# Optimization experiments

Hardware: AMD Instinct MI355X
Metric: run time of the kernel (lower is better)

Reference implementation:

```python
import jax, jax.numpy as jnp
import numpy as np

V_SIZE, E, H = 30000, 256, 128   # vocab, emb_dim, GRU hidden per direction
B, U, T, ND = 32, 32, 128, 64    # dialogues, utterances, max tokens, dialogue-id table size
SCALE = E ** 0.5                  # attention normalise_factor = hid_size**0.5, hid_size = emb_dim


def _gru_dir(x_seq, w_ih, w_hh, b_ih, b_hh):
    """Unidirectional torch-style GRU. x_seq: [N,T,E] -> [N,T,H]."""
    xp = jnp.einsum('nte,ge->ntg', x_seq, w_ih) + b_ih   # precompute input gates [N,T,3H]
    xp = jnp.swapaxes(xp, 0, 1)                          # [T,N,3H]

    def step(h, xpt):
        gh = h @ w_hh.T + b_hh
        r = jax.nn.sigmoid(xpt[:, :H] + gh[:, :H])
        z = jax.nn.sigmoid(xpt[:, H:2 * H] + gh[:, H:2 * H])
        n = jnp.tanh(xpt[:, 2 * H:] + r * gh[:, 2 * H:])
        h_new = (1.0 - z) * n + z * h
        return h_new, h_new

    h0 = jnp.zeros((x_seq.shape[0], H), x_seq.dtype)
    _, out = jax.lax.scan(step, h0, xp)
    return jnp.swapaxes(out, 0, 1)


def _forward(x, d_ids, utt_len, emb_table,
             w_ih_f, w_hh_f, b_ih_f, b_hh_f,
             w_ih_b, w_hh_b, b_ih_b, b_hh_b,
             wq, bq, wk, bk, wv, bv, wo, bo, wl, bl):
    b, u, t = x.shape
    N = b * u
    emb = emb_table[x.reshape(N, t)]                      # [N,T,E]
    lens = jnp.clip(utt_len[d_ids].reshape(N), 1, t)      # valid tokens per utterance
    pos = jnp.arange(t)
    # index map that reverses the valid prefix (padding region clipped, unused)
    rev_idx = jnp.clip(lens[:, None] - 1 - pos[None, :], 0, t - 1)  # [N,T]

    o_f = _gru_dir(emb, w_ih_f, w_hh_f, b_ih_f, b_hh_f)   # causal => correct on valid prefix
    emb_rev = jnp.take_along_axis(emb, rev_idx[:, :, None], axis=1)
    o_b = jnp.take_along_axis(_gru_dir(emb_rev, w_ih_b, w_hh_b, b_ih_b, b_hh_b),
                              rev_idx[:, :, None], axis=1)
    h = jnp.concatenate([o_f, o_b], axis=-1)              # [N,T,E] bi-GRU states

    # self-attention pooling; original takes op[-1], so only the query at the
    # last valid token (lens-1) is needed -- identical math, less compute.
    k = jnp.einsum('nte,he->nth', h, wk) + bk
    v = jnp.einsum('nte,he->nth', h, wv) + bv
    h_last = jnp.take_along_axis(h, (lens - 1)[:, None, None], axis=1)[:, 0]  # [N,E]
    q = h_last @ wq.T + bq
    score = jnp.einsum('nh,nth->nt', q, k) / SCALE
    score = jnp.where(pos[None, :] < lens[:, None], score, -jnp.inf)
    attn = jax.nn.softmax(score, axis=-1)
    ctx = jnp.einsum('nt,nth->nh', attn, v)
    out = (ctx @ wo.T + bo) @ wl.T + bl                   # make_output then final linear
    return out.reshape(b, u, -1)


def setup_inputs() -> dict:
    key = jax.random.key(0)
    ks = jax.random.split(key, 16)

    def p(k, shape):
        return (jax.random.normal(k, shape, jnp.float32) / np.sqrt(shape[-1])).astype(jnp.float32)

    return {
        'x': jax.random.randint(ks[0], (B, U, T), 0, V_SIZE, dtype=jnp.int32),
        'd_ids': jax.random.randint(ks[1], (B,), 0, ND, dtype=jnp.int32),
        'utt_len': jax.random.randint(ks[2], (ND, U), 1, T + 1, dtype=jnp.int32),
        'emb_table': p(ks[3], (V_SIZE, E)),
        'w_ih_f': p(ks[4], (3 * H, E)), 'w_hh_f': p(ks[5], (3 * H, H)),
        'b_ih_f': jnp.zeros(3 * H, jnp.float32), 'b_hh_f': jnp.zeros(3 * H, jnp.float32),
        'w_ih_b': p(ks[6], (3 * H, E)), 'w_hh_b': p(ks[7], (3 * H, H)),
        'b_ih_b': jnp.zeros(3 * H, jnp.float32), 'b_hh_b': jnp.zeros(3 * H, jnp.float32),
        'wq': p(ks[8], (E, E)), 'bq': jnp.zeros(E, jnp.float32),
        'wk': p(ks[9], (E, E)), 'bk': jnp.zeros(E, jnp.float32),
        'wv': p(ks[10], (E, E)), 'bv': jnp.zeros(E, jnp.float32),
        'wo': p(ks[11], (E, E)), 'bo': jnp.zeros(E, jnp.float32),
        'wl': p(ks[12], (E, E)), 'bl': jnp.zeros(E, jnp.float32),
    }


def reference(x, d_ids, utt_len, emb_table,
              w_ih_f, w_hh_f, b_ih_f, b_hh_f,
              w_ih_b, w_hh_b, b_ih_b, b_hh_b,
              wq, bq, wk, bk, wv, bv, wo, bo, wl, bl):
    return _forward(x, d_ids, utt_len, emb_table,
                    w_ih_f, w_hh_f, b_ih_f, b_hh_f,
                    w_ih_b, w_hh_b, b_ih_b, b_hh_b,
                    wq, bq, wk, bk, wv, bv, wo, bo, wl, bl)
```

## Files before the change

### kernel.cpp

```cpp
#include <hip/hip_runtime.h>
#include <hip/hip_bf16.h>
#include <math.h>
#include <stdint.h>

typedef unsigned short u16;
typedef unsigned int   u32;
typedef __attribute__((ext_vector_type(8))) short bf16x8;
typedef __attribute__((ext_vector_type(4))) float f32x4;

#define EDIM 256
#define HDIM 128
#define TLEN 128
#define NUTT 1024
#define UU   32
#define NBU  8

#define WS_FLAG 0
#define WS_LENS 64
#define WS_TAB  4608
#define WS_COPY 8192
#define WS_OF   18874368LL
#define WS_OB   52428800LL

#define MFMA16(a, b, c) __builtin_amdgcn_mfma_f32_16x16x32_bf16((a), (b), (c), 0, 0, 0)
#define SOUT(u, s, j) ((u) * 1096 + (s) * 136 + (j))

__constant__ int G_SZ[18] = {7680000, 98304, 49152, 384, 384, 98304, 49152, 384, 384,
                             65536, 256, 65536, 65536, 256, 65536, 256, 65536, 256};

__device__ __forceinline__ float b2f(u16 b) {
    u32 u = ((u32)b) << 16; float f; __builtin_memcpy(&f, &u, 4); return f;
}
__device__ __forceinline__ u16 f2b(float f) {
    u32 u; __builtin_memcpy(&u, &f, 4);
    u32 r = u + 0x7FFFu + ((u >> 16) & 1u);
    return (u16)(r >> 16);
}
__device__ __forceinline__ u16 f2b_hw(float f) {
    __hip_bfloat16 h = __float2bfloat16(f);
    u16 v; __builtin_memcpy(&v, &h, 2); return v;
}
__device__ __forceinline__ float fsigmoid(float x) { return 1.0f / (1.0f + __expf(-x)); }
__device__ __forceinline__ float ftanh(float x) { return 1.0f - 2.0f / (__expf(2.0f * x) + 1.0f); }

__global__ __launch_bounds__(256)
void k_convert(void* ws,
               const int* __restrict__ d_ids, const int* __restrict__ utt_len,
               const void* a0, const void* a1, const void* a2, const void* a3,
               const void* a4, const void* a5, const void* a6, const void* a7,
               const void* a8, const void* a9, const void* a10, const void* a11,
               const void* a12, const void* a13, const void* a14, const void* a15,
               const void* a16, const void* a17) {
    __shared__ int scnt[4];
    const int tid = threadIdx.x, lane = tid & 63, wid = tid >> 6;
    const u16* p = (const u16*)a0;
    int cnt = 0;
#pragma unroll 8
    for (int i = tid; i < 16384; i += 256)
        cnt += ((p[i] & 0x7F80) == 0x7F80) ? 1 : 0;
#pragma unroll
    for (int o = 32; o > 0; o >>= 1) cnt += __shfl_down(cnt, o);
    if (lane == 0) scnt[wid] = cnt;
    __syncthreads();
    const int flag = (scnt[0] + scnt[1] + scnt[2] + scnt[3] > 0) ? 1 : 0;

    if (blockIdx.x == 0) {
        if (tid == 0) {
            const void* orig[18] = {a0,a1,a2,a3,a4,a5,a6,a7,a8,a9,a10,a11,a12,a13,a14,a15,a16,a17};
            *(int*)((char*)ws + WS_FLAG) = flag;
            const u16** tab = (const u16**)((char*)ws + WS_TAB);
            char* base = (char*)ws + WS_COPY;
            long long cum = 0;
            for (int a = 0; a < 18; ++a) {
                tab[a] = flag ? (const u16*)(base + cum * 2) : (const u16*)orig[a];
                cum += G_SZ[a];
            }
        }
        int* lens = (int*)((char*)ws + WS_LENS);
#pragma unroll 4
        for (int n = tid; n < NUTT; n += 256) {
            int b = n >> 5;
            int u = n & (UU - 1);
            int L = utt_len[d_ids[b] * UU + u];
            lens[n] = min(max(L, 1), TLEN);
        }
    }

    if (flag == 0) return;
    const void* orig[18] = {a0,a1,a2,a3,a4,a5,a6,a7,a8,a9,a10,a11,a12,a13,a14,a15,a16,a17};
    u16* base = (u16*)((char*)ws + WS_COPY);
    const int gtid = blockIdx.x * blockDim.x + tid;
    const int gs   = gridDim.x * blockDim.x;
    long long cum = 0;
    for (int a = 0; a < 18; ++a) {
        const float4* src = (const float4*)orig[a];
        uint2* dst = (uint2*)(base + cum);
        const int n4 = G_SZ[a] >> 2;
        for (int i = gtid; i < n4; i += gs) {
            float4 v = src[i];
            uint2 pk;
            pk.x = (u32)f2b(v.x) | ((u32)f2b(v.y) << 16);
            pk.y = (u32)f2b(v.z) | ((u32)f2b(v.w) << 16);
            dst[i] = pk;
        }
        cum += G_SZ[a];
    }
}

__global__ __launch_bounds__(512)
void k_scan(const int* __restrict__ x, void* ws) {
    const u16* const* tab = (const u16* const*)((char*)ws + WS_TAB);
    const int dir = blockIdx.y;
    const u16* emb  = tab[0];
    const u16* w_ih = tab[1 + dir * 4];
    const u16* w_hh = tab[2 + dir * 4];
    const u16* b_ih = tab[3 + dir * 4];
    const u16* b_hh = tab[4 + dir * 4];
    u16* outp = (u16*)((char*)ws + (dir ? WS_OB : WS_OF));
    const int* lens = (const int*)((char*)ws + WS_LENS);

    const int n0 = blockIdx.x * NBU;
    __shared__ __align__(16) u16 sh_emb[2][NBU][264];
    __shared__ __align__(16) u16 sh_hi[2][NBU * 136];
    __shared__ __align__(16) u16 sh_lo[2][NBU * 136];
    __shared__ __align__(16) u16 sh_out[2][NBU * 1096];
    __shared__ int sh_tok[NBU * TLEN];
    __shared__ int sh_L[NBU];

    const int tid = threadIdx.x, lane = tid & 63, wvi = tid >> 6;
    const int q4 = lane >> 4, mm = lane & 15;
    const int j = wvi * 16 + mm;
    const int u8 = mm & 7;

    for (int i = tid; i < NBU * 136; i += 512) { sh_hi[0][i] = 0; sh_lo[0][i] = 0; }
    for (int i = tid; i < NBU * TLEN; i += 512) {
        const int u = i >> 7, tt = i & 127;
        sh_tok[i] = x[(n0 + u) * TLEN + tt];
    }
    if (tid < NBU) sh_L[tid] = lens[n0 + tid];

    bf16x8 wih[3][8]; bf16x8 whh[3][4];
    float bcr, bcz, bxn, bgn;
#pragma unroll
    for (int n3 = 0; n3 < 3; ++n3) {
        const int g = n3 * HDIM + j;
#pragma unroll
        for (int ks = 0; ks < 8; ++ks)
            wih[n3][ks] = *(const bf16x8*)(w_ih + g * EDIM + ks * 32 + q4 * 8);
#pragma unroll
        for (int ks = 0; ks < 4; ++ks)
            whh[n3][ks] = *(const bf16x8*)(w_hh + g * HDIM + ks * 32 + q4 * 8);
    }
    bcr = b2f(b_ih[j]) + b2f(b_hh[j]);
    bcz = b2f(b_ih[HDIM + j]) + b2f(b_hh[HDIM + j]);
    bxn = b2f(b_ih[2 * HDIM + j]);
    bgn = b2f(b_hh[2 * HDIM + j]);

    const int arr0 = (q4 & 2);
    float hprev[2] = {0.f, 0.f};
    const f32x4 zero4 = {0.f, 0.f, 0.f, 0.f};
    __syncthreads();

    const bool pwave = (wvi < 4);
    const int pf_u = lane & 7;
    const int pf_c = wvi * 8 + (lane >> 3);
    const int pf_L = sh_L[pf_u];

    uint4 pf;
    if (pwave) {
        const int te0 = dir ? (pf_L - 1) : 0;
        const int tok = sh_tok[pf_u * TLEN + te0];
        pf = *(const uint4*)(emb + (size_t)tok * EDIM + pf_c * 8);
        *(uint4*)&sh_emb[0][pf_u][pf_c * 8] = pf;
    }
    __syncthreads();

    for (int t = 0; t < TLEN; ++t) {
        const int cur = t & 1, nxt = cur ^ 1;
        const int obuf = (t >> 3) & 1, slot = t & 7;

        if (pwave && (t + 1 < TLEN)) {
            const int te = dir ? max(pf_L - 2 - t, 0) : (t + 1);
            const int tok = sh_tok[pf_u * TLEN + te];
            pf = *(const uint4*)(emb + (size_t)tok * EDIM + pf_c * 8);
        }

        f32x4 accx[3], accg[3];
        {
            bf16x8 a = *(const bf16x8*)&sh_emb[cur][u8][q4 * 8];
#pragma unroll
            for (int n3 = 0; n3 < 3; ++n3) accx[n3] = MFMA16(a, wih[n3][0], zero4);
        }
#pragma unroll
        for (int ks = 1; ks < 8; ++ks) {
            bf16x8 a = *(const bf16x8*)&sh_emb[cur][u8][ks * 32 + q4 * 8];
#pragma unroll
            for (int n3 = 0; n3 < 3; ++n3) accx[n3] = MFMA16(a, wih[n3][ks], accx[n3]);
        }
        {
            bf16x8 ahi = *(const bf16x8*)(sh_hi[cur] + u8 * 136 + q4 * 8);
            bf16x8 alo = *(const bf16x8*)(sh_lo[cur] + u8 * 136 + q4 * 8);
#pragma unroll
            for (int n3 = 0; n3 < 3; ++n3) {
                accg[n3] = MFMA16(ahi, whh[n3][0], zero4);
                accg[n3] = MFMA16(alo, whh[n3][0], accg[n3]);
            }
        }
#pragma unroll
        for (int ks = 1; ks < 4; ++ks) {
            bf16x8 ahi = *(const bf16x8*)(sh_hi[cur] + u8 * 136 + ks * 32 + q4 * 8);
            bf16x8 alo = *(const bf16x8*)(sh_lo[cur] + u8 * 136 + ks * 32 + q4 * 8);
#pragma unroll
            for (int n3 = 0; n3 < 3; ++n3) {
                accg[n3] = MFMA16(ahi, whh[n3][ks], accg[n3]);
                accg[n3] = MFMA16(alo, whh[n3][ks], accg[n3]);
            }
        }

#pragma unroll
        for (int rr2 = 0; rr2 < 2; ++rr2) {
            const int arr = rr2 + arr0;
            const int u   = (q4 * 4 + arr) & 7;
            const float r  = fsigmoid(accx[0][arr] + accg[0][arr] + bcr);
            const float z  = fsigmoid(accx[1][arr] + accg[1][arr] + bcz);
            const float nn = ftanh((accx[2][arr] + bxn) + r * (accg[2][arr] + bgn));
            const float hn = (1.0f - z) * nn + z * hprev[rr2];
            hprev[rr2] = hn;
            const u16 hb = f2b_hw(hn);
            sh_hi[nxt][u * 136 + j] = hb;
            sh_lo[nxt][u * 136 + j] = f2b_hw(hn - b2f(hb));
            sh_out[obuf][SOUT(u, slot, j)] = hb;
        }

        if (pwave && (t + 1 < TLEN))
            *(uint4*)&sh_emb[nxt][pf_u][pf_c * 8] = pf;

        __syncthreads();

        if (slot == 7) {
            const int rowIdx = tid >> 3;
            const int part   = tid & 7;
            const int fu = rowIdx >> 3, fs = rowIdx & 7;
            const int tt = (t & ~7) + fs;
            const int tout = dir ? (sh_L[fu] - 1 - tt) : tt;
            if (tout >= 0) {
                const u16* srcp = &sh_out[obuf][SOUT(fu, fs, part * 16)];
                uint4 v0 = *(const uint4*)(srcp);
                uint4 v1 = *(const uint4*)(srcp + 8);
                u16* dstp = outp + ((size_t)(n0 + fu) * TLEN + tout) * HDIM + part * 16;
                *(uint4*)(dstp)     = v0;
                *(uint4*)(dstp + 8) = v1;
            }
        }
    }
}

__global__ __launch_bounds__(256)
void k_attn(void* ws, void* outv) {
    const u16* const* tab = (const u16* const*)((char*)ws + WS_TAB);
    const u16* wq = tab[9];  const u16* bq = tab[10];
    const u16* wk = tab[11];
    const u16* wv = tab[12]; const u16* bv = tab[13];
    const u16* wo = tab[14]; const u16* bo = tab[15];
    const u16* wl = tab[16]; const u16* bl = tab[17];
    const int* lens = (const int*)((char*)ws + WS_LENS);
    const int flag = *(const int*)((const char*)ws + WS_FLAG);

    const int n = blockIdx.x;
    const int L = lens[n];
    const u16* hf = (const u16*)((char*)ws + WS_OF) + (size_t)n * TLEN * HDIM;
    const u16* hb = (const u16*)((char*)ws + WS_OB) + (size_t)n * TLEN * HDIM;

    __shared__ float sh_hl[EDIM];
    __shared__ float sh_v1[EDIM];
    __shared__ float sh_uv[EDIM];
    __shared__ float sh_a[4 * EDIM];
    __shared__ float sh_m[4], sh_l[4];

    const int tid = threadIdx.x, lane = tid & 63, wid = tid >> 6;

    sh_hl[tid] = (tid < HDIM) ? b2f(hf[(size_t)(L - 1) * HDIM + tid])
                              : b2f(hb[(size_t)(L - 1) * HDIM + (tid - HDIM)]);
    __syncthreads();

    {
        float s0 = b2f(bq[tid]), s1 = 0.0f;
        const u16* wr = wq + tid * EDIM;
#pragma unroll
        for (int ks = 0; ks < 32; ks += 2) {
            bf16x8 w8 = *(const bf16x8*)(wr + ks * 8);
            bf16x8 w9 = *(const bf16x8*)(wr + ks * 8 + 8);
#pragma unroll
            for (int d = 0; d < 8; ++d) {
                s0 += b2f((u16)w8[d]) * sh_hl[ks * 8 + d];
                s1 += b2f((u16)w9[d]) * sh_hl[ks * 8 + 8 + d];
            }
        }
        sh_v1[tid] = s0 + s1;
    }
    __syncthreads();

    {
        float s0 = 0.0f, s1 = 0.0f;
        for (int i = 0; i < EDIM; i += 2) {
            s0 += b2f(wk[i * EDIM + tid]) * sh_v1[i];
            s1 += b2f(wk[(i + 1) * EDIM + tid]) * sh_v1[i + 1];
        }
        sh_uv[tid] = s0 + s1;
    }
    __syncthreads();

    {
        const int e0 = lane * 4;
        const float u0 = sh_uv[e0], u1 = sh_uv[e0 + 1];
        const float u2 = sh_uv[e0 + 2], u3 = sh_uv[e0 + 3];
        float m = -1e30f, l = 0.0f;
        float a0 = 0.f, a1 = 0.f, a2 = 0.f, a3 = 0.f;
        for (int t = wid; t < L; t += 4) {
            const u16* src = (lane < 32) ? (hf + (size_t)t * HDIM + lane * 4)
                                         : (hb + (size_t)t * HDIM + (lane - 32) * 4);
            uint2 pv = *(const uint2*)src;
            const float h0 = b2f((u16)(pv.x & 0xFFFF));
            const float h1 = b2f((u16)(pv.x >> 16));
            const float h2 = b2f((u16)(pv.y & 0xFFFF));
            const float h3 = b2f((u16)(pv.y >> 16));
            float p = h0 * u0 + h1 * u1 + h2 * u2 + h3 * u3;
#pragma unroll
            for (int o = 32; o > 0; o >>= 1) p += __shfl_xor(p, o);
            const float s = p * 0.0625f;
            const float mn = fmaxf(m, s);
            const float c = __expf(m - mn);
            const float w = __expf(s - mn);
            l = l * c + w;
            a0 = a0 * c + w * h0;
            a1 = a1 * c + w * h1;
            a2 = a2 * c + w * h2;
            a3 = a3 * c + w * h3;
            m = mn;
        }
        sh_a[wid * EDIM + e0]     = a0;
        sh_a[wid * EDIM + e0 + 1] = a1;
        sh_a[wid * EDIM + e0 + 2] = a2;
        sh_a[wid * EDIM + e0 + 3] = a3;
        if (lane == 0) { sh_m[wid] = m; sh_l[wid] = l; }
    }
    __syncthreads();

    {
        const float m0 = sh_m[0], m1 = sh_m[1], m2 = sh_m[2], m3 = sh_m[3];
        const float M = fmaxf(fmaxf(m0, m1), fmaxf(m2, m3));
        const float c0 = __expf(m0 - M), c1 = __expf(m1 - M);
        const float c2 = __expf(m2 - M), c3 = __expf(m3 - M);
        const float den = c0 * sh_l[0] + c1 * sh_l[1] + c2 * sh_l[2] + c3 * sh_l[3];
        const float num = c0 * sh_a[tid] + c1 * sh_a[EDIM + tid] +
                          c2 * sh_a[2 * EDIM + tid] + c3 * sh_a[3 * EDIM + tid];
        sh_hl[tid] = num / den;
    }
    __syncthreads();

    {
        float s0 = b2f(bv[tid]), s1 = 0.0f;
        const u16* wr = wv + tid * EDIM;
#pragma unroll
        for (int ks = 0; ks < 32; ks += 2) {
            bf16x8 w8 = *(const bf16x8*)(wr + ks * 8);
            bf16x8 w9 = *(const bf16x8*)(wr + ks * 8 + 8);
#pragma unroll
            for (int d = 0; d < 8; ++d) {
                s0 += b2f((u16)w8[d]) * sh_hl[ks * 8 + d];
                s1 += b2f((u16)w9[d]) * sh_hl[ks * 8 + 8 + d];
            }
        }
        sh_uv[tid] = s0 + s1;
    }
    __syncthreads();

    {
        float s0 = b2f(bo[tid]), s1 = 0.0f;
        const u16* wr = wo + tid * EDIM;
#pragma unroll
        for (int ks = 0; ks < 32; ks += 2) {
            bf16x8 w8 = *(const bf16x8*)(wr + ks * 8);
            bf16x8 w9 = *(const bf16x8*)(wr + ks * 8 + 8);
#pragma unroll
            for (int d = 0; d < 8; ++d) {
                s0 += b2f((u16)w8[d]) * sh_uv[ks * 8 + d];
                s1 += b2f((u16)w9[d]) * sh_uv[ks * 8 + 8 + d];
            }
        }
        sh_v1[tid] = s0 + s1;
    }
    __syncthreads();

    {
        float s0 = b2f(bl[tid]), s1 = 0.0f;
        const u16* wr = wl + tid * EDIM;
#pragma unroll
        for (int ks = 0; ks < 32; ks += 2) {
            bf16x8 w8 = *(const bf16x8*)(wr + ks * 8);
            bf16x8 w9 = *(const bf16x8*)(wr + ks * 8 + 8);
#pragma unroll
            for (int d = 0; d < 8; ++d) {
                s0 += b2f((u16)w8[d]) * sh_v1[ks * 8 + d];
                s1 += b2f((u16)w9[d]) * sh_v1[ks * 8 + 8 + d];
            }
        }
        const float s = s0 + s1;
        const size_t oidx = (size_t)n * EDIM + tid;
        if (flag) ((float*)outv)[oidx] = s;
        else      ((u16*)outv)[oidx]   = f2b(s);
    }
}

extern "C" void kernel_launch(void* const* d_in, const int* in_sizes, int n_in,
                              void* d_out, int out_size, void* d_ws, size_t ws_size,
                              hipStream_t stream) {
    const int* x       = (const int*)d_in[0];
    const int* d_ids   = (const int*)d_in[1];
    const int* utt_len = (const int*)d_in[2];
    const void* f_arr[18] = {
        d_in[3],
        d_in[4], d_in[5], d_in[6], d_in[7],
        d_in[8], d_in[9], d_in[10], d_in[11],
        d_in[12], d_in[13],
        d_in[14],
        d_in[16], d_in[17],
        d_in[18], d_in[19],
        d_in[20], d_in[21]
    };

    k_convert<<<512, 256, 0, stream>>>(d_ws, d_ids, utt_len,
        f_arr[0], f_arr[1], f_arr[2], f_arr[3], f_arr[4], f_arr[5], f_arr[6], f_arr[7],
        f_arr[8], f_arr[9], f_arr[10], f_arr[11], f_arr[12], f_arr[13], f_arr[14],
        f_arr[15], f_arr[16], f_arr[17]);

    k_scan<<<dim3(NUTT / NBU, 2), 512, 0, stream>>>(x, d_ws);

    k_attn<<<NUTT, 256, 0, stream>>>(d_ws, d_out);
}
```

Baseline: 399.0 us.

## Split GRU scan into input-projection and recurrence waves with one-step lookahead

The scan block grows to 1024 threads. Eight waves now compute the input projection for step t+1 into a shared-memory double buffer, while the other eight waves run the recurrent matmul and gate math for step t. This takes the input-gate MFMAs off the serial recurrence critical path and halves the weight registers each wave holds, at the cost of extra shared memory and a 1024-thread block. Separately, the attention pooling loop handles two timesteps per iteration with a merged online-softmax update to get more memory-level parallelism.

```diff
diff --git a/kernel.cpp b/kernel.cpp
--- a/kernel.cpp
+++ b/kernel.cpp
@@ -24,6 +24,7 @@
 
 #define MFMA16(a, b, c) __builtin_amdgcn_mfma_f32_16x16x32_bf16((a), (b), (c), 0, 0, 0)
 #define SOUT(u, s, j) ((u) * 1096 + (s) * 136 + (j))
+#define XP(buf, u, g) ((buf) * (NBU * 392) + (u) * 392 + (g))
 
 __constant__ int G_SZ[18] = {7680000, 98304, 49152, 384, 384, 98304, 49152, 384, 384,
                              65536, 256, 65536, 65536, 256, 65536, 256, 65536, 256};
@@ -107,7 +108,7 @@
     }
 }
 
-__global__ __launch_bounds__(512)
+__global__ __launch_bounds__(1024)
 void k_scan(const int* __restrict__ x, void* ws) {
     const u16* const* tab = (const u16* const*)((char*)ws + WS_TAB);
     const int dir = blockIdx.y;
@@ -124,54 +125,95 @@
     __shared__ __align__(16) u16 sh_hi[2][NBU * 136];
     __shared__ __align__(16) u16 sh_lo[2][NBU * 136];
     __shared__ __align__(16) u16 sh_out[2][NBU * 1096];
+    __shared__ float sh_xp[2 * NBU * 392];
     __shared__ int sh_tok[NBU * TLEN];
     __shared__ int sh_L[NBU];
 
     const int tid = threadIdx.x, lane = tid & 63, wvi = tid >> 6;
+    const bool xw = (wvi < 8);
+    const int w  = xw ? wvi : (wvi - 8);
     const int q4 = lane >> 4, mm = lane & 15;
-    const int j = wvi * 16 + mm;
+    const int j  = w * 16 + mm;
     const int u8 = mm & 7;
-
-    for (int i = tid; i < NBU * 136; i += 512) { sh_hi[0][i] = 0; sh_lo[0][i] = 0; }
-    for (int i = tid; i < NBU * TLEN; i += 512) {
-        const int u = i >> 7, tt = i & 127;
-        sh_tok[i] = x[(n0 + u) * TLEN + tt];
+    const int arr0 = q4 & 2;
+    const int u0_ = (q4 * 4 + arr0) & 7;
+    const int u1_ = (q4 * 4 + arr0 + 1) & 7;
+
+    for (int i = tid; i < NBU * 136; i += 1024) { sh_hi[0][i] = 0; sh_lo[0][i] = 0; }
+    {
+        const int u = tid >> 7, tt = tid & 127;
+        sh_tok[tid] = x[(n0 + u) * TLEN + tt];
     }
     if (tid < NBU) sh_L[tid] = lens[n0 + tid];
 
-    bf16x8 wih[3][8]; bf16x8 whh[3][4];
-    float bcr, bcz, bxn, bgn;
-#pragma unroll
-    for (int n3 = 0; n3 < 3; ++n3) {
-        const int g = n3 * HDIM + j;
-#pragma unroll
-        for (int ks = 0; ks < 8; ++ks)
-            wih[n3][ks] = *(const bf16x8*)(w_ih + g * EDIM + ks * 32 + q4 * 8);
-#pragma unroll
-        for (int ks = 0; ks < 4; ++ks)
-            whh[n3][ks] = *(const bf16x8*)(w_hh + g * HDIM + ks * 32 + q4 * 8);
-    }
-    bcr = b2f(b_ih[j]) + b2f(b_hh[j]);
-    bcz = b2f(b_ih[HDIM + j]) + b2f(b_hh[HDIM + j]);
-    bxn = b2f(b_ih[2 * HDIM + j]);
-    bgn = b2f(b_hh[2 * HDIM + j]);
-
-    const int arr0 = (q4 & 2);
-    float hprev[2] = {0.f, 0.f};
+    bf16x8 W[3][8];
+    if (xw) {
+#pragma unroll
+        for (int n3 = 0; n3 < 3; ++n3) {
+            const int g = n3 * HDIM + j;
+#pragma unroll
+            for (int ks = 0; ks < 8; ++ks)
+                W[n3][ks] = *(const bf16x8*)(w_ih + g * EDIM + ks * 32 + q4 * 8);
+        }
+    } else {
+#pragma unroll
+        for (int n3 = 0; n3 < 3; ++n3) {
+            const int g = n3 * HDIM + j;
+#pragma unroll
+            for (int ks = 0; ks < 4; ++ks)
+                W[n3][ks] = *(const bf16x8*)(w_hh + g * HDIM + ks * 32 + q4 * 8);
+        }
+    }
+    float bcr = 0.f, bcz = 0.f, bxn = 0.f, bgn = 0.f;
+    float hprev0 = 0.f, hprev1 = 0.f;
+    if (!xw) {
+        bcr = b2f(b_ih[j]) + b2f(b_hh[j]);
+        bcz = b2f(b_ih[HDIM + j]) + b2f(b_hh[HDIM + j]);
+        bxn = b2f(b_ih[2 * HDIM + j]);
+        bgn = b2f(b_hh[2 * HDIM + j]);
+    }
     const f32x4 zero4 = {0.f, 0.f, 0.f, 0.f};
     __syncthreads();
 
-    const bool pwave = (wvi < 4);
+    const int f_part = tid & 15;
+    const int f_u = tid >> 7, f_s = (tid >> 4) & 7;
+    const int f_L = sh_L[f_u];
+
+    const bool pw = xw && (wvi < 4);
     const int pf_u = lane & 7;
     const int pf_c = wvi * 8 + (lane >> 3);
     const int pf_L = sh_L[pf_u];
-
-    uint4 pf;
-    if (pwave) {
+    const int Lu0 = sh_L[u0_], Lu1 = sh_L[u1_];
+
+    if (pw) {
         const int te0 = dir ? (pf_L - 1) : 0;
-        const int tok = sh_tok[pf_u * TLEN + te0];
-        pf = *(const uint4*)(emb + (size_t)tok * EDIM + pf_c * 8);
+        uint4 pf = *(const uint4*)(emb + (size_t)sh_tok[pf_u * TLEN + te0] * EDIM + pf_c * 8);
         *(uint4*)&sh_emb[0][pf_u][pf_c * 8] = pf;
+    }
+    __syncthreads();
+    if (xw) {
+        f32x4 acc[3];
+        {
+            bf16x8 a = *(const bf16x8*)&sh_emb[0][u8][q4 * 8];
+#pragma unroll
+            for (int n3 = 0; n3 < 3; ++n3) acc[n3] = MFMA16(a, W[n3][0], zero4);
+        }
+#pragma unroll
+        for (int ks = 1; ks < 8; ++ks) {
+            bf16x8 a = *(const bf16x8*)&sh_emb[0][u8][ks * 32 + q4 * 8];
+#pragma unroll
+            for (int n3 = 0; n3 < 3; ++n3) acc[n3] = MFMA16(a, W[n3][ks], acc[n3]);
+        }
+#pragma unroll
+        for (int n3 = 0; n3 < 3; ++n3) {
+            sh_xp[XP(0, u0_, n3 * HDIM + j)] = acc[n3][arr0];
+            sh_xp[XP(0, u1_, n3 * HDIM + j)] = acc[n3][arr0 + 1];
+        }
+        if (pw) {
+            const int te1 = dir ? max(pf_L - 2, 0) : 1;
+            uint4 pf = *(const uint4*)(emb + (size_t)sh_tok[pf_u * TLEN + te1] * EDIM + pf_c * 8);
+            *(uint4*)&sh_emb[1][pf_u][pf_c * 8] = pf;
+        }
     }
     __syncthreads();
 
@@ -179,77 +221,93 @@
         const int cur = t & 1, nxt = cur ^ 1;
         const int obuf = (t >> 3) & 1, slot = t & 7;
 
-        if (pwave && (t + 1 < TLEN)) {
-            const int te = dir ? max(pf_L - 2 - t, 0) : (t + 1);
-            const int tok = sh_tok[pf_u * TLEN + te];
-            pf = *(const uint4*)(emb + (size_t)tok * EDIM + pf_c * 8);
-        }
-
-        f32x4 accx[3], accg[3];
-        {
-            bf16x8 a = *(const bf16x8*)&sh_emb[cur][u8][q4 * 8];
-#pragma unroll
-            for (int n3 = 0; n3 < 3; ++n3) accx[n3] = MFMA16(a, wih[n3][0], zero4);
-        }
-#pragma unroll
-        for (int ks = 1; ks < 8; ++ks) {
-            bf16x8 a = *(const bf16x8*)&sh_emb[cur][u8][ks * 32 + q4 * 8];
-#pragma unroll
-            for (int n3 = 0; n3 < 3; ++n3) accx[n3] = MFMA16(a, wih[n3][ks], accx[n3]);
-        }
-        {
-            bf16x8 ahi = *(const bf16x8*)(sh_hi[cur] + u8 * 136 + q4 * 8);
-            bf16x8 alo = *(const bf16x8*)(sh_lo[cur] + u8 * 136 + q4 * 8);
-#pragma unroll
-            for (int n3 = 0; n3 < 3; ++n3) {
-                accg[n3] = MFMA16(ahi, whh[n3][0], zero4);
-                accg[n3] = MFMA16(alo, whh[n3][0], accg[n3]);
-            }
-        }
-#pragma unroll
-        for (int ks = 1; ks < 4; ++ks) {
-            bf16x8 ahi = *(const bf16x8*)(sh_hi[cur] + u8 * 136 + ks * 32 + q4 * 8);
-            bf16x8 alo = *(const bf16x8*)(sh_lo[cur] + u8 * 136 + ks * 32 + q4 * 8);
-#pragma unroll
-            for (int n3 = 0; n3 < 3; ++n3) {
-                accg[n3] = MFMA16(ahi, whh[n3][ks], accg[n3]);
-                accg[n3] = MFMA16(alo, whh[n3][ks], accg[n3]);
-            }
-        }
-
-#pragma unroll
-        for (int rr2 = 0; rr2 < 2; ++rr2) {
-            const int arr = rr2 + arr0;
-            const int u   = (q4 * 4 + arr) & 7;
-            const float r  = fsigmoid(accx[0][arr] + accg[0][arr] + bcr);
-            const float z  = fsigmoid(accx[1][arr] + accg[1][arr] + bcz);
-            const float nn = ftanh((accx[2][arr] + bxn) + r * (accg[2][arr] + bgn));
-            const float hn = (1.0f - z) * nn + z * hprev[rr2];
-            hprev[rr2] = hn;
-            const u16 hb = f2b_hw(hn);
-            sh_hi[nxt][u * 136 + j] = hb;
-            sh_lo[nxt][u * 136 + j] = f2b_hw(hn - b2f(hb));
-            sh_out[obuf][SOUT(u, slot, j)] = hb;
-        }
-
-        if (pwave && (t + 1 < TLEN))
-            *(uint4*)&sh_emb[nxt][pf_u][pf_c * 8] = pf;
-
+        if (xw) {
+            uint4 pf;
+            const bool dopf = pw && (t + 2 < TLEN);
+            if (dopf) {
+                const int te = dir ? max(pf_L - 3 - t, 0) : (t + 2);
+                pf = *(const uint4*)(emb + (size_t)sh_tok[pf_u * TLEN + te] * EDIM + pf_c * 8);
+            }
+            if (t + 1 < TLEN) {
+                f32x4 acc[3];
+                {
+                    bf16x8 a = *(const bf16x8*)&sh_emb[nxt][u8][q4 * 8];
+#pragma unroll
+                    for (int n3 = 0; n3 < 3; ++n3) acc[n3] = MFMA16(a, W[n3][0], zero4);
+                }
+#pragma unroll
+                for (int ks = 1; ks < 8; ++ks) {
+                    bf16x8 a = *(const bf16x8*)&sh_emb[nxt][u8][ks * 32 + q4 * 8];
+#pragma unroll
+                    for (int n3 = 0; n3 < 3; ++n3) acc[n3] = MFMA16(a, W[n3][ks], acc[n3]);
+                }
+#pragma unroll
+                for (int n3 = 0; n3 < 3; ++n3) {
+                    sh_xp[XP(nxt, u0_, n3 * HDIM + j)] = acc[n3][arr0];
+                    sh_xp[XP(nxt, u1_, n3 * HDIM + j)] = acc[n3][arr0 + 1];
+                }
+            }
+            if (dopf)
+                *(uint4*)&sh_emb[cur][pf_u][pf_c * 8] = pf;
+        } else {
+            const float xr0 = sh_xp[XP(cur, u0_, j)];
+            const float xz0 = sh_xp[XP(cur, u0_, HDIM + j)];
+            const float xn0 = sh_xp[XP(cur, u0_, 2 * HDIM + j)];
+            const float xr1 = sh_xp[XP(cur, u1_, j)];
+            const float xz1 = sh_xp[XP(cur, u1_, HDIM + j)];
+            const float xn1 = sh_xp[XP(cur, u1_, 2 * HDIM + j)];
+
+            f32x4 acc[3];
+            {
+                bf16x8 ahi = *(const bf16x8*)(sh_hi[cur] + u8 * 136 + q4 * 8);
+                bf16x8 alo = *(const bf16x8*)(sh_lo[cur] + u8 * 136 + q4 * 8);
+#pragma unroll
+                for (int n3 = 0; n3 < 3; ++n3) {
+                    acc[n3] = MFMA16(ahi, W[n3][0], zero4);
+                    acc[n3] = MFMA16(alo, W[n3][0], acc[n3]);
+                }
+            }
+#pragma unroll
+            for (int ks = 1; ks < 4; ++ks) {
+                bf16x8 ahi = *(const bf16x8*)(sh_hi[cur] + u8 * 136 + ks * 32 + q4 * 8);
+                bf16x8 alo = *(const bf16x8*)(sh_lo[cur] + u8 * 136 + ks * 32 + q4 * 8);
+#pragma unroll
+                for (int n3 = 0; n3 < 3; ++n3) {
+                    acc[n3] = MFMA16(ahi, W[n3][ks], acc[n3]);
+                    acc[n3] = MFMA16(alo, W[n3][ks], acc[n3]);
+                }
+            }
+            {
+                const float r  = fsigmoid(xr0 + acc[0][arr0] + bcr);
+                const float z  = fsigmoid(xz0 + acc[1][arr0] + bcz);
+                const float nn = ftanh((xn0 + bxn) + r * (acc[2][arr0] + bgn));
+                const float hn = (1.0f - z) * nn + z * hprev0;
+                hprev0 = hn;
+                const u16 hb = f2b_hw(hn);
+                sh_hi[nxt][u0_ * 136 + j] = hb;
+                sh_lo[nxt][u0_ * 136 + j] = f2b_hw(hn - b2f(hb));
+                sh_out[obuf][SOUT(u0_, slot, j)] = hb;
+            }
+            {
+                const float r  = fsigmoid(xr1 + acc[0][arr0 + 1] + bcr);
+                const float z  = fsigmoid(xz1 + acc[1][arr0 + 1] + bcz);
+                const float nn = ftanh((xn1 + bxn) + r * (acc[2][arr0 + 1] + bgn));
+                const float hn = (1.0f - z) * nn + z * hprev1;
+                hprev1 = hn;
+                const u16 hb = f2b_hw(hn);
+                sh_hi[nxt][u1_ * 136 + j] = hb;
+                sh_lo[nxt][u1_ * 136 + j] = f2b_hw(hn - b2f(hb));
+                sh_out[obuf][SOUT(u1_, slot, j)] = hb;
+            }
+        }
         __syncthreads();
 
         if (slot == 7) {
-            const int rowIdx = tid >> 3;
-            const int part   = tid & 7;
-            const int fu = rowIdx >> 3, fs = rowIdx & 7;
-            const int tt = (t & ~7) + fs;
-            const int tout = dir ? (sh_L[fu] - 1 - tt) : tt;
+            const int tt = (t & ~7) + f_s;
+            const int tout = dir ? (f_L - 1 - tt) : tt;
             if (tout >= 0) {
-                const u16* srcp = &sh_out[obuf][SOUT(fu, fs, part * 16)];
-                uint4 v0 = *(const uint4*)(srcp);
-                uint4 v1 = *(const uint4*)(srcp + 8);
-                u16* dstp = outp + ((size_t)(n0 + fu) * TLEN + tout) * HDIM + part * 16;
-                *(uint4*)(dstp)     = v0;
-                *(uint4*)(dstp + 8) = v1;
+                uint4 v = *(const uint4*)&sh_out[obuf][SOUT(f_u, f_s, f_part * 8)];
+                *(uint4*)(outp + ((size_t)(n0 + f_u) * TLEN + tout) * HDIM + f_part * 8) = v;
             }
         }
     }
@@ -314,28 +372,54 @@
         const int e0 = lane * 4;
         const float u0 = sh_uv[e0], u1 = sh_uv[e0 + 1];
         const float u2 = sh_uv[e0 + 2], u3 = sh_uv[e0 + 3];
+        const size_t off = (lane < 32) ? ((size_t)lane * 4)
+                                       : ((size_t)(lane - 32) * 4);
+        const u16* basep = (lane < 32) ? hf : hb;
         float m = -1e30f, l = 0.0f;
         float a0 = 0.f, a1 = 0.f, a2 = 0.f, a3 = 0.f;
-        for (int t = wid; t < L; t += 4) {
-            const u16* src = (lane < 32) ? (hf + (size_t)t * HDIM + lane * 4)
-                                         : (hb + (size_t)t * HDIM + (lane - 32) * 4);
-            uint2 pv = *(const uint2*)src;
-            const float h0 = b2f((u16)(pv.x & 0xFFFF));
-            const float h1 = b2f((u16)(pv.x >> 16));
-            const float h2 = b2f((u16)(pv.y & 0xFFFF));
-            const float h3 = b2f((u16)(pv.y >> 16));
+        int t = wid;
+        for (; t + 4 < L; t += 8) {
+            uint2 pA = *(const uint2*)(basep + (size_t)t * HDIM + off);
+            uint2 pB = *(const uint2*)(basep + (size_t)(t + 4) * HDIM + off);
+            const float hA0 = b2f((u16)(pA.x & 0xFFFF)), hA1 = b2f((u16)(pA.x >> 16));
+            const float hA2 = b2f((u16)(pA.y & 0xFFFF)), hA3 = b2f((u16)(pA.y >> 16));
+            const float hB0 = b2f((u16)(pB.x & 0xFFFF)), hB1 = b2f((u16)(pB.x >> 16));
+            const float hB2 = b2f((u16)(pB.y & 0xFFFF)), hB3 = b2f((u16)(pB.y >> 16));
+            float pa = hA0 * u0 + hA1 * u1 + hA2 * u2 + hA3 * u3;
+            float pb = hB0 * u0 + hB1 * u1 + hB2 * u2 + hB3 * u3;
+#pragma unroll
+            for (int o = 32; o > 0; o >>= 1) {
+                pa += __shfl_xor(pa, o);
+                pb += __shfl_xor(pb, o);
+            }
+            const float s1v = pa * 0.0625f, s2v = pb * 0.0625f;
+            const float mn = fmaxf(m, fmaxf(s1v, s2v));
+            const float c  = __expf(m - mn);
+            const float w1 = __expf(s1v - mn);
+            const float w2 = __expf(s2v - mn);
+            l = l * c + w1 + w2;
+            a0 = a0 * c + w1 * hA0 + w2 * hB0;
+            a1 = a1 * c + w1 * hA1 + w2 * hB1;
+            a2 = a2 * c + w1 * hA2 + w2 * hB2;
+            a3 = a3 * c + w1 * hA3 + w2 * hB3;
+            m = mn;
+        }
+        if (t < L) {
+            uint2 pv = *(const uint2*)(basep + (size_t)t * HDIM + off);
+            const float h0 = b2f((u16)(pv.x & 0xFFFF)), h1 = b2f((u16)(pv.x >> 16));
+            const float h2 = b2f((u16)(pv.y & 0xFFFF)), h3 = b2f((u16)(pv.y >> 16));
             float p = h0 * u0 + h1 * u1 + h2 * u2 + h3 * u3;
 #pragma unroll
             for (int o = 32; o > 0; o >>= 1) p += __shfl_xor(p, o);
             const float s = p * 0.0625f;
             const float mn = fmaxf(m, s);
             const float c = __expf(m - mn);
-            const float w = __expf(s - mn);
-            l = l * c + w;
-            a0 = a0 * c + w * h0;
-            a1 = a1 * c + w * h1;
-            a2 = a2 * c + w * h2;
-            a3 = a3 * c + w * h3;
+            const float wv_ = __expf(s - mn);
+            l = l * c + wv_;
+            a0 = a0 * c + wv_ * h0;
+            a1 = a1 * c + wv_ * h1;
+            a2 = a2 * c + wv_ * h2;
+            a3 = a3 * c + wv_ * h3;
             m = mn;
         }
         sh_a[wid * EDIM + e0]     = a0;
@@ -434,7 +518,7 @@
         f_arr[8], f_arr[9], f_arr[10], f_arr[11], f_arr[12], f_arr[13], f_arr[14],
         f_arr[15], f_arr[16], f_arr[17]);
 
-    k_scan<<<dim3(NUTT / NBU, 2), 512, 0, stream>>>(x, d_ws);
+    k_scan<<<dim3(NUTT / NBU, 2), 1024, 0, stream>>>(x, d_ws);
 
     k_attn<<<NUTT, 256, 0, stream>>>(d_ws, d_out);
 }
```

Measured after the change: 641.1 us. 1.61x slower.
